# Kernel optimization log

Hardware: AMD Instinct MI355X
Metric: run time of the kernel (lower is better)

## Reference

```python
import jax, jax.numpy as jnp
import numpy as np
from jax import lax

B, S, H = 2, 1024, 1024
I = 512            # moe_intermediate_size
E = 32             # n_routed_experts
TOP_K = 4
N_GROUP = 4
TOPK_GROUP = 2
SCALE = 2.5        # routed_scaling_factor
N_SHARED = 2
SH_I = I * N_SHARED


def setup_inputs() -> dict:
    key = jax.random.key(0)
    ks = jax.random.split(key, 10)
    std = 0.02
    return {
        "hidden_states": jax.random.normal(ks[0], (B, S, H), jnp.float32),
        "router_weight": jax.random.normal(ks[1], (E, H), jnp.float32) * std,
        "router_bias": jnp.zeros((E,), jnp.float32),
        "gate_w": jax.random.normal(ks[2], (E, I, H), jnp.float32) * std,
        "up_w": jax.random.normal(ks[3], (E, I, H), jnp.float32) * std,
        "down_w": jax.random.normal(ks[4], (E, H, I), jnp.float32) * std,
        "shared_gate_w": jax.random.normal(ks[5], (SH_I, H), jnp.float32) * std,
        "shared_up_w": jax.random.normal(ks[6], (SH_I, H), jnp.float32) * std,
        "shared_down_w": jax.random.normal(ks[7], (H, SH_I), jnp.float32) * std,
    }


def _route(tokens, router_weight, router_bias):
    # tokens: [T, H] -> topk_idx [T, K] int, topk_weight [T, K] f32
    logits = tokens.astype(jnp.float32) @ router_weight.astype(jnp.float32).T  # [T, E]
    scores = jax.nn.sigmoid(logits)
    sfc = scores + router_bias[None, :]
    T = tokens.shape[0]
    # group scores: sum of top-2 per group
    grp = sfc.reshape(T, N_GROUP, E // N_GROUP)
    group_scores = lax.top_k(grp, 2)[0].sum(-1)                 # [T, n_group]
    _, gidx = lax.top_k(group_scores, TOPK_GROUP)               # [T, topk_group]
    gmask = jax.nn.one_hot(gidx, N_GROUP, dtype=sfc.dtype).sum(1)  # [T, n_group]
    smask = jnp.broadcast_to(gmask[:, :, None], (T, N_GROUP, E // N_GROUP)).reshape(T, E)
    tmp = jnp.where(smask > 0, sfc, 0.0)
    _, topk_idx = lax.top_k(tmp, TOP_K)                         # [T, K]
    topk_w = jnp.take_along_axis(scores, topk_idx, axis=1)
    topk_w = topk_w / (topk_w.sum(-1, keepdims=True) + 1e-20)   # norm_topk_prob
    topk_w = topk_w * SCALE
    return topk_idx, topk_w


def reference(hidden_states, router_weight, router_bias, gate_w, up_w, down_w,
              shared_gate_w, shared_up_w, shared_down_w):
    tokens = hidden_states.reshape(-1, H)                       # [T, H]
    topk_idx, topk_w = _route(tokens, router_weight, router_bias)
    # dense all-expert SwiGLU
    gate_vals = jax.nn.silu(jnp.einsum('th,eih->tei', tokens, gate_w))
    up_vals = jnp.einsum('th,eih->tei', tokens, up_w)
    hidden_vals = gate_vals * up_vals                           # [T, E, I]
    expert_out = jnp.einsum('tei,ehi->teh', hidden_vals, down_w)  # [T, E, H]
    sel = jnp.take_along_axis(expert_out, topk_idx[:, :, None], axis=1)  # [T, K, H]
    mixed = (sel * topk_w[:, :, None].astype(sel.dtype)).sum(1)
    mixed = mixed.reshape(hidden_states.shape)
    # shared experts (dense SwiGLU MLP)
    sg = jax.nn.silu(jnp.einsum('bsh,ih->bsi', hidden_states, shared_gate_w))
    su = jnp.einsum('bsh,ih->bsi', hidden_states, shared_up_w)
    shared = jnp.einsum('bsi,hi->bsh', sg * su, shared_down_w)
    return mixed + shared
```

## Files before the change

### kernel.cpp

```cpp
#include <hip/hip_runtime.h>
#include <hip/hip_bf16.h>
#include <math.h>

#define HD 1024
#define ID 512
#define NE 32
#define NT 2048
#define NG 4
#define SHI 1024
#define SCALE 2.5f

#define BN 64
#define BK 32
#define LDA 40
#define NCV 4

typedef __bf16 bf16_t;
typedef __attribute__((ext_vector_type(8))) __bf16 bf16x8;
typedef __attribute__((ext_vector_type(4))) __bf16 bf16x4;
typedef __attribute__((ext_vector_type(4))) float f32x4;

__device__ __forceinline__ void gld16(const bf16_t* g, bf16_t* l) {
    __builtin_amdgcn_global_load_lds(
        (__attribute__((address_space(1))) void*)g,
        (__attribute__((address_space(3))) void*)l,
        16, 0, 0);
}

__device__ __forceinline__ void cvt16(const float* __restrict__ src, bf16_t* __restrict__ dst) {
    float4 a0 = ((const float4*)src)[0], a1 = ((const float4*)src)[1];
    float4 a2 = ((const float4*)src)[2], a3 = ((const float4*)src)[3];
    bf16x8 o0, o1;
    o0[0]=(__bf16)a0.x; o0[1]=(__bf16)a0.y; o0[2]=(__bf16)a0.z; o0[3]=(__bf16)a0.w;
    o0[4]=(__bf16)a1.x; o0[5]=(__bf16)a1.y; o0[6]=(__bf16)a1.z; o0[7]=(__bf16)a1.w;
    o1[0]=(__bf16)a2.x; o1[1]=(__bf16)a2.y; o1[2]=(__bf16)a2.z; o1[3]=(__bf16)a2.w;
    o1[4]=(__bf16)a3.x; o1[5]=(__bf16)a3.y; o1[6]=(__bf16)a3.z; o1[7]=(__bf16)a3.w;
    ((bf16x8*)dst)[0] = o0;
    ((bf16x8*)dst)[1] = o1;
}

__global__ void __launch_bounds__(256) convert_A(
    const float* __restrict__ g, const float* __restrict__ u,
    const float* __restrict__ sg, const float* __restrict__ su,
    const float* __restrict__ hs, bf16_t* __restrict__ dst,
    float* __restrict__ outz)
{
    const long long UG = (long long)NE * ID * HD / 16;
    const long long US = (long long)SHI * HD / 16;
    const long long UH = (long long)NT * HD / 16;
    const long long TOTC = 2 * UG + 2 * US + UH;
    const long long TOT = TOTC + UH;
    for (long long c = blockIdx.x * 256LL + threadIdx.x; c < TOT;
         c += (long long)gridDim.x * 256LL) {
        if (c >= TOTC) {
            long long r = c - TOTC;
            float4 z = {0.f, 0.f, 0.f, 0.f};
            float4* p = (float4*)(outz + r * 16);
            p[0] = z; p[1] = z; p[2] = z; p[3] = z;
            continue;
        }
        const float* src;
        long long r = c;
        if (r < UG)                   src = g  + r * 16;
        else if ((r -= UG) < UG)      src = u  + r * 16;
        else if ((r -= UG) < US)      src = sg + r * 16;
        else if ((r -= US) < US)      src = su + r * 16;
        else { r -= US;               src = hs + r * 16; }
        cvt16(src, dst + c * 16);
    }
}

#define LTOK 8
#define LKC 64
__global__ void __launch_bounds__(256) logits_kernel(
    const float* __restrict__ hs, const float* __restrict__ rw,
    float* __restrict__ logits, int* __restrict__ counts)
{
    if (blockIdx.x == 0 && threadIdx.x < NE) counts[threadIdx.x] = 0;

    __shared__ float Xs[LTOK][68];
    __shared__ float Ws[NE][65];

    int tid = threadIdx.x;
    int t0 = blockIdx.x * LTOK;
    int tslot = tid >> 5, ecol = tid & 31;
    float acc = 0.f;

    for (int k0 = 0; k0 < HD; k0 += LKC) {
        if (tid < 128) {
            int row = tid >> 4, q = tid & 15;
            float4 v = *(const float4*)(hs + (size_t)(t0 + row) * HD + k0 + q * 4);
            *(float4*)(&Xs[row][q * 4]) = v;
        }
        #pragma unroll
        for (int i = 0; i < 8; ++i) {
            int idx = i * 256 + tid;
            int e = idx >> 6, kk = idx & 63;
            Ws[e][kk] = rw[(size_t)e * HD + k0 + kk];
        }
        __syncthreads();
        #pragma unroll 8
        for (int kk = 0; kk < LKC; ++kk)
            acc += Xs[tslot][kk] * Ws[ecol][kk];
        __syncthreads();
    }
    logits[(size_t)(t0 + tslot) * NE + ecol] = acc;
}

__global__ void __launch_bounds__(256) topk_kernel(
    const float* __restrict__ logits, const float* __restrict__ rb,
    float* __restrict__ topkw, int* __restrict__ counts, int* __restrict__ lists)
{
    int t = blockIdx.x * 256 + threadIdx.x;
    if (t >= NT) return;

    float scores[NE], sfc[NE], tmp[NE];
    #pragma unroll
    for (int e = 0; e < NE; ++e) {
        float l = logits[(size_t)t * NE + e];
        float s = 1.f / (1.f + __expf(-l));
        scores[e] = s;
        sfc[e] = s + rb[e];
    }
    float gs[NG];
    #pragma unroll
    for (int g = 0; g < NG; ++g) {
        float m1 = -1e30f, m2 = -1e30f;
        #pragma unroll
        for (int j = 0; j < 8; ++j) {
            float v = sfc[g * 8 + j];
            if (v > m1) { m2 = m1; m1 = v; } else if (v > m2) m2 = v;
        }
        gs[g] = m1 + m2;
    }
    int g1 = 0;
    #pragma unroll
    for (int g = 1; g < NG; ++g) if (gs[g] > gs[g1]) g1 = g;
    int g2 = -1;
    #pragma unroll
    for (int g = 0; g < NG; ++g) {
        if (g == g1) continue;
        if (g2 < 0 || gs[g] > gs[g2]) g2 = g;
    }
    #pragma unroll
    for (int e = 0; e < NE; ++e) {
        int g = e >> 3;
        tmp[e] = (g == g1 || g == g2) ? sfc[e] : 0.0f;
    }
    int idx[4]; float wk[4]; float wsum = 0.f;
    #pragma unroll
    for (int k = 0; k < 4; ++k) {
        int best = 0; float bv = -1e30f;
        #pragma unroll
        for (int e = 0; e < NE; ++e) if (tmp[e] > bv) { bv = tmp[e]; best = e; }
        idx[k] = best; tmp[best] = -1e30f;
        wk[k] = scores[best]; wsum += wk[k];
    }
    float inv = SCALE / (wsum + 1e-20f);
    #pragma unroll
    for (int k = 0; k < 4; ++k) {
        int p = t * 4 + k;
        topkw[p] = wk[k] * inv;
        int e = idx[k];
        int pos = atomicAdd(&counts[e], 1);
        lists[e * NT + pos] = p;
    }
}


__global__ void __launch_bounds__(256) gateup_all(
    const bf16_t* __restrict__ hs_b,
    const bf16_t* __restrict__ wg_b, const bf16_t* __restrict__ wu_b,
    const bf16_t* __restrict__ sg_b, const bf16_t* __restrict__ su_b,
    bf16_t* __restrict__ hr, bf16_t* __restrict__ hsh,
    const int* __restrict__ lists, const int* __restrict__ counts,
    const float* __restrict__ dwf, const float* __restrict__ sdwf,
    bf16_t* __restrict__ dstB)
{
    int bx = blockIdx.x, mtb = blockIdx.y, zz = blockIdx.z;
    int tid = threadIdx.x;

    if (bx >= 34) {
        const long long UD = (long long)NE * HD * ID / 16;
        const long long USD = (long long)HD * SHI / 16;
        const long long TOT = UD + USD;
        long long c = (((long long)(bx - 34) * 16 + mtb) * 8 + zz) * 256 + tid;
        const long long stride = (long long)NCV * 128 * 256;
        for (; c < TOT; c += stride) {
            const float* src = (c < UD) ? (dwf + c * 16) : (sdwf + (c - UD) * 16);
            cvt16(src, dstB + c * 16);
        }
        return;
    }

    constexpr int BMT = 128, NB = 64;
    constexpr int AU = 2, MT = 4;

    int cnt, ntb, ND;
    const bf16_t *wg, *wu;
    bf16_t* hout;
    const int* rlist = nullptr;
    if (bx < 32) {
        int e = bx; cnt = counts[e];
        if (mtb * BMT >= cnt) return;
        ntb = zz;
        wg = wg_b + (size_t)e * ID * HD;
        wu = wu_b + (size_t)e * ID * HD;
        hout = hr; ND = ID;
        rlist = lists + e * NT;
    } else {
        cnt = NT;
        ntb = (bx - 32) * 8 + zz;
        wg = sg_b; wu = su_b;
        hout = hsh; ND = SHI;
    }

    __shared__ __align__(16) bf16_t As[2][BMT * BK];
    __shared__ __align__(16) bf16_t Bgs[2][NB * BK];
    __shared__ __align__(16) bf16_t Bus[2][NB * BK];
    __shared__ int rowid[BMT];

    if (tid < BMT) {
        int gm = mtb * BMT + tid;
        int mm = gm < cnt ? gm : cnt - 1;
        rowid[tid] = rlist ? rlist[mm] : mm;
    }
    __syncthreads();

    int lane = tid & 63;
    int w = tid >> 6;
    int wm = w & 1, wn = w >> 1;
    int lrow = lane & 15, quad = lane >> 4, chunkL = lane & 3;

    const bf16_t* asrc[AU];
    #pragma unroll
    for (int i = 0; i < AU; ++i) {
        int row = (w * AU + i) * 16 + (lane >> 2);
        int tok = rlist ? (rowid[row] >> 2) : rowid[row];
        int ch = chunkL ^ ((row >> 1) & 3);
        asrc[i] = hs_b + (size_t)tok * HD + ch * 8;
    }
    int nrow = w * 16 + (lane >> 2);
    int nch = chunkL ^ ((nrow >> 1) & 3);
    const bf16_t* bgsrc = wg + (size_t)(ntb * NB + nrow) * HD + nch * 8;
    const bf16_t* busrc = wu + (size_t)(ntb * NB + nrow) * HD + nch * 8;

    int aoff[MT], goff[2];
    #pragma unroll
    for (int mt = 0; mt < MT; ++mt) {
        int row = wm * (BMT / 2) + mt * 16 + lrow;
        aoff[mt] = row * BK + (quad ^ ((row >> 1) & 3)) * 8;
    }
    #pragma unroll
    for (int nt = 0; nt < 2; ++nt) {
        int row = wn * 32 + nt * 16 + lrow;
        goff[nt] = row * BK + (quad ^ ((row >> 1) & 3)) * 8;
    }

    f32x4 accg[MT][2], accu[MT][2];
    #pragma unroll
    for (int i = 0; i < MT; ++i)
        #pragma unroll
        for (int j = 0; j < 2; ++j) { accg[i][j] = (f32x4){0,0,0,0}; accu[i][j] = (f32x4){0,0,0,0}; }

    auto stage = [&](int buf, int k) {
        #pragma unroll
        for (int i = 0; i < AU; ++i)
            gld16(asrc[i] + k, &As[buf][(w * AU + i) * 512]);
        gld16(bgsrc + k, &Bgs[buf][w * 512]);
        gld16(busrc + k, &Bus[buf][w * 512]);
    };
    auto compute = [&](int buf) {
        bf16x8 af[MT], bg[2], bu[2];
        #pragma unroll
        for (int mt = 0; mt < MT; ++mt) af[mt] = *(const bf16x8*)(&As[buf][aoff[mt]]);
        #pragma unroll
        for (int nt = 0; nt < 2; ++nt) {
            bg[nt] = *(const bf16x8*)(&Bgs[buf][goff[nt]]);
            bu[nt] = *(const bf16x8*)(&Bus[buf][goff[nt]]);
        }
        #pragma unroll
        for (int mt = 0; mt < MT; ++mt)
            #pragma unroll
            for (int nt = 0; nt < 2; ++nt) {
                accg[mt][nt] = __builtin_amdgcn_mfma_f32_16x16x32_bf16(af[mt], bg[nt], accg[mt][nt], 0, 0, 0);
                accu[mt][nt] = __builtin_amdgcn_mfma_f32_16x16x32_bf16(af[mt], bu[nt], accu[mt][nt], 0, 0, 0);
            }
    };

    stage(0, 0);
    __syncthreads();
    int buf = 0;
    for (int k0 = BK; k0 < HD; k0 += BK) {
        stage(buf ^ 1, k0);
        compute(buf);
        __syncthreads();
        buf ^= 1;
    }
    compute(buf);

    #pragma unroll
    for (int mt = 0; mt < MT; ++mt)
        #pragma unroll
        for (int r = 0; r < 4; ++r) {
            int row_local = wm * (BMT / 2) + mt * 16 + quad * 4 + r;
            int gm = mtb * BMT + row_local;
            if (gm >= cnt) continue;
            int p = rowid[row_local];
            #pragma unroll
            for (int nt = 0; nt < 2; ++nt) {
                int col = ntb * NB + wn * 32 + nt * 16 + lrow;
                float gv = accg[mt][nt][r], uv = accu[mt][nt][r];
                float h = (gv / (1.f + __expf(-gv))) * uv;
                hout[(size_t)p * ND + col] = (__bf16)h;
            }
        }
}

__global__ void __launch_bounds__(256) down_all(
    const bf16_t* __restrict__ hr, const bf16_t* __restrict__ hsh,
    const bf16_t* __restrict__ wd_b, const bf16_t* __restrict__ sd_b,
    float* __restrict__ out,
    const int* __restrict__ lists, const int* __restrict__ counts,
    const float* __restrict__ topkw)
{
    int bx = blockIdx.x, mtb = blockIdx.y, zz = blockIdx.z;
    int tid = threadIdx.x;

    constexpr int BMT = 128, NB = 64;
    constexpr int AU = 2, MT = 4;

    int cnt, ntb, KD;
    const bf16_t *Hin, *wd;
    const int* rlist = nullptr;
    bool routed;
    if (bx < 64) {
        int e = bx >> 1; cnt = counts[e];
        if (mtb * BMT >= cnt) return;
        ntb = (bx & 1) * 8 + zz;
        Hin = hr; wd = wd_b + (size_t)e * HD * ID; KD = ID;
        rlist = lists + e * NT;
        routed = true;
    } else {
        cnt = NT;
        ntb = (bx - 64) * 8 + zz;
        Hin = hsh; wd = sd_b; KD = SHI;
        routed = false;
    }

    __shared__ __align__(16) bf16_t As[2][BMT * BK];
    __shared__ __align__(16) bf16_t Ws[2][NB * BK];
    __shared__ int rowid[BMT];

    if (tid < BMT) {
        int gm = mtb * BMT + tid;
        int mm = gm < cnt ? gm : cnt - 1;
        rowid[tid] = rlist ? rlist[mm] : mm;
    }
    __syncthreads();

    int lane = tid & 63;
    int w = tid >> 6;
    int wm = w & 1, wn = w >> 1;
    int lrow = lane & 15, quad = lane >> 4, chunkL = lane & 3;

    const bf16_t* asrc[AU];
    #pragma unroll
    for (int i = 0; i < AU; ++i) {
        int row = (w * AU + i) * 16 + (lane >> 2);
        int ch = chunkL ^ ((row >> 1) & 3);
        asrc[i] = Hin + (size_t)rowid[row] * KD + ch * 8;
    }
    int nrow = w * 16 + (lane >> 2);
    int nch = chunkL ^ ((nrow >> 1) & 3);
    const bf16_t* wsrc = wd + (size_t)(ntb * NB + nrow) * KD + nch * 8;

    int aoff[MT], woff[2];
    #pragma unroll
    for (int mt = 0; mt < MT; ++mt) {
        int row = wm * (BMT / 2) + mt * 16 + lrow;
        aoff[mt] = row * BK + (quad ^ ((row >> 1) & 3)) * 8;
    }
    #pragma unroll
    for (int nt = 0; nt < 2; ++nt) {
        int row = wn * 32 + nt * 16 + lrow;
        woff[nt] = row * BK + (quad ^ ((row >> 1) & 3)) * 8;
    }

    f32x4 acc[MT][2];
    #pragma unroll
    for (int i = 0; i < MT; ++i)
        #pragma unroll
        for (int j = 0; j < 2; ++j) acc[i][j] = (f32x4){0,0,0,0};

    auto stage = [&](int buf, int k) {
        #pragma unroll
        for (int i = 0; i < AU; ++i)
            gld16(asrc[i] + k, &As[buf][(w * AU + i) * 512]);
        gld16(wsrc + k, &Ws[buf][w * 512]);
    };
    auto compute = [&](int buf) {
        bf16x8 af[MT], br[2];
        #pragma unroll
        for (int mt = 0; mt < MT; ++mt) af[mt] = *(const bf16x8*)(&As[buf][aoff[mt]]);
        #pragma unroll
        for (int nt = 0; nt < 2; ++nt) br[nt] = *(const bf16x8*)(&Ws[buf][woff[nt]]);
        #pragma unroll
        for (int mt = 0; mt < MT; ++mt)
            #pragma unroll
            for (int nt = 0; nt < 2; ++nt)
                acc[mt][nt] = __builtin_amdgcn_mfma_f32_16x16x32_bf16(af[mt], br[nt], acc[mt][nt], 0, 0, 0);
    };

    stage(0, 0);
    __syncthreads();
    int buf = 0;
    for (int k0 = BK; k0 < KD; k0 += BK) {
        stage(buf ^ 1, k0);
        compute(buf);
        __syncthreads();
        buf ^= 1;
    }
    compute(buf);

    #pragma unroll
    for (int mt = 0; mt < MT; ++mt)
        #pragma unroll
        for (int r = 0; r < 4; ++r) {
            int row_local = wm * (BMT / 2) + mt * 16 + quad * 4 + r;
            int gm = mtb * BMT + row_local;
            if (gm >= cnt) continue;
            int p = rowid[row_local];
            #pragma unroll
            for (int nt = 0; nt < 2; ++nt) {
                int col = ntb * NB + wn * 32 + nt * 16 + lrow;
                float val = acc[mt][nt][r];
                if (routed) {
                    float wgt = topkw[p];
                    atomicAdd(&out[(size_t)(p >> 2) * HD + col], wgt * val);
                } else {
                    atomicAdd(&out[(size_t)p * HD + col], val);
                }
            }
        }
}


__device__ inline bf16x4 cvt4(float4 v) {
    bf16x4 r;
    r[0] = (__bf16)v.x; r[1] = (__bf16)v.y; r[2] = (__bf16)v.z; r[3] = (__bf16)v.w;
    return r;
}

template<bool EXPERT, int ND, int BMT>
__global__ void __launch_bounds__(256) gateup_mfma(
    const float* __restrict__ X, const float* __restrict__ Wg,
    const float* __restrict__ Wu, bf16_t* __restrict__ Hout,
    const int* __restrict__ lists, const int* __restrict__ counts)
{
    int e = 0, cnt = NT;
    const float* wg = Wg; const float* wu = Wu;
    if (EXPERT) {
        e = blockIdx.x; cnt = counts[e];
        wg = Wg + (size_t)e * ND * HD;
        wu = Wu + (size_t)e * ND * HD;
    }
    int mtb = blockIdx.y, ntb = blockIdx.z;
    if (mtb * BMT >= cnt) return;

    __shared__ __align__(16) bf16_t As[BMT * LDA];
    __shared__ __align__(16) bf16_t Bgs[BN * LDA];
    __shared__ __align__(16) bf16_t Bus[BN * LDA];
    __shared__ int rowid[BMT];

    int tid = threadIdx.x;
    if (tid < BMT) {
        int gm = mtb * BMT + tid;
        int mm = gm < cnt ? gm : cnt - 1;
        rowid[tid] = EXPERT ? lists[e * NT + mm] : mm;
    }
    __syncthreads();

    constexpr int AR = (BMT * BK) / (256 * 4);
    constexpr int BR = (BN * BK) / (256 * 4);
    constexpr int MT = BMT / 32;

    int lane = tid & 63;
    int w = tid >> 6;
    int wm = w & 1, wn = w >> 1;
    int lrow = lane & 15, quad = lane >> 4;

    f32x4 accg[MT][2], accu[MT][2];
    #pragma unroll
    for (int i = 0; i < MT; ++i)
        #pragma unroll
        for (int j = 0; j < 2; ++j) { accg[i][j] = (f32x4){0,0,0,0}; accu[i][j] = (f32x4){0,0,0,0}; }

    float4 pa[AR], pbg[BR], pbu[BR];

    #pragma unroll
    for (int r = 0; r < AR; ++r) {
        int idx = r * 256 + tid;
        int row = idx >> 3, kq = idx & 7;
        int tok = EXPERT ? (rowid[row] >> 2) : rowid[row];
        pa[r] = *(const float4*)(X + (size_t)tok * HD + kq * 4);
    }
    #pragma unroll
    for (int r = 0; r < BR; ++r) {
        int idx = r * 256 + tid;
        int n = idx >> 3, kq = idx & 7;
        size_t off = (size_t)(ntb * BN + n) * HD + kq * 4;
        pbg[r] = *(const float4*)(wg + off);
        pbu[r] = *(const float4*)(wu + off);
    }

    for (int k0 = 0; k0 < HD; k0 += BK) {
        #pragma unroll
        for (int r = 0; r < AR; ++r) {
            int idx = r * 256 + tid;
            int row = idx >> 3, kq = idx & 7;
            *(bf16x4*)(As + row * LDA + kq * 4) = cvt4(pa[r]);
        }
        #pragma unroll
        for (int r = 0; r < BR; ++r) {
            int idx = r * 256 + tid;
            int n = idx >> 3, kq = idx & 7;
            *(bf16x4*)(Bgs + n * LDA + kq * 4) = cvt4(pbg[r]);
            *(bf16x4*)(Bus + n * LDA + kq * 4) = cvt4(pbu[r]);
        }
        __syncthreads();

        int k1 = k0 + BK;
        if (k1 < HD) {
            #pragma unroll
            for (int r = 0; r < AR; ++r) {
                int idx = r * 256 + tid;
                int row = idx >> 3, kq = idx & 7;
                int tok = EXPERT ? (rowid[row] >> 2) : rowid[row];
                pa[r] = *(const float4*)(X + (size_t)tok * HD + k1 + kq * 4);
            }
            #pragma unroll
            for (int r = 0; r < BR; ++r) {
                int idx = r * 256 + tid;
                int n = idx >> 3, kq = idx & 7;
                size_t off = (size_t)(ntb * BN + n) * HD + k1 + kq * 4;
                pbg[r] = *(const float4*)(wg + off);
                pbu[r] = *(const float4*)(wu + off);
            }
        }

        bf16x8 af[MT], bg[2], bu[2];
        #pragma unroll
        for (int mt = 0; mt < MT; ++mt)
            af[mt] = *(const bf16x8*)(As + (wm * (BMT / 2) + mt * 16 + lrow) * LDA + quad * 8);
        #pragma unroll
        for (int nt = 0; nt < 2; ++nt) {
            bg[nt] = *(const bf16x8*)(Bgs + (wn * 32 + nt * 16 + lrow) * LDA + quad * 8);
            bu[nt] = *(const bf16x8*)(Bus + (wn * 32 + nt * 16 + lrow) * LDA + quad * 8);
        }
        #pragma unroll
        for (int mt = 0; mt < MT; ++mt)
            #pragma unroll
            for (int nt = 0; nt < 2; ++nt) {
                accg[mt][nt] = __builtin_amdgcn_mfma_f32_16x16x32_bf16(af[mt], bg[nt], accg[mt][nt], 0, 0, 0);
                accu[mt][nt] = __builtin_amdgcn_mfma_f32_16x16x32_bf16(af[mt], bu[nt], accu[mt][nt], 0, 0, 0);
            }
        __syncthreads();
    }

    #pragma unroll
    for (int mt = 0; mt < MT; ++mt)
        #pragma unroll
        for (int r = 0; r < 4; ++r) {
            int row_local = wm * (BMT / 2) + mt * 16 + quad * 4 + r;
            int gm = mtb * BMT + row_local;
            if (gm >= cnt) continue;
            int p = rowid[row_local];
            #pragma unroll
            for (int nt = 0; nt < 2; ++nt) {
                int col = ntb * BN + wn * 32 + nt * 16 + lrow;
                float g = accg[mt][nt][r], u = accu[mt][nt][r];
                float h = (g / (1.f + __expf(-g))) * u;
                Hout[(size_t)p * ND + col] = (__bf16)h;
            }
        }
}

template<bool EXPERT, int KD, int BMT>
__global__ void __launch_bounds__(256) down_mfma(
    const bf16_t* __restrict__ Hin, const float* __restrict__ Wd,
    float* __restrict__ out, const int* __restrict__ lists,
    const int* __restrict__ counts, const float* __restrict__ topkw)
{
    int e = 0, cnt = NT;
    const float* wd = Wd;
    if (EXPERT) {
        e = blockIdx.x; cnt = counts[e];
        wd = Wd + (size_t)e * HD * KD;
    }
    int mtb = blockIdx.y, ntb = blockIdx.z;
    if (mtb * BMT >= cnt) return;

    __shared__ __align__(16) bf16_t As[BMT * LDA];
    __shared__ __align__(16) bf16_t Ws[BN * LDA];
    __shared__ int rowid[BMT];

    int tid = threadIdx.x;
    if (tid < BMT) {
        int gm = mtb * BMT + tid;
        int mm = gm < cnt ? gm : cnt - 1;
        rowid[tid] = EXPERT ? lists[e * NT + mm] : mm;
    }
    __syncthreads();

    constexpr int ARH = (BMT * BK / 8) / 256;
    constexpr int BR = (BN * BK) / (256 * 4);
    constexpr int MT = BMT / 32;

    int lane = tid & 63;
    int w = tid >> 6;
    int wm = w & 1, wn = w >> 1;
    int lrow = lane & 15, quad = lane >> 4;

    f32x4 acc[MT][2];
    #pragma unroll
    for (int i = 0; i < MT; ++i)
        #pragma unroll
        for (int j = 0; j < 2; ++j) acc[i][j] = (f32x4){0,0,0,0};

    bf16x8 pa[ARH];
    float4 pw[BR];

    #pragma unroll
    for (int r = 0; r < ARH; ++r) {
        int idx = r * 256 + tid;
        int row = idx >> 2, c = idx & 3;
        pa[r] = *(const bf16x8*)(Hin + (size_t)rowid[row] * KD + c * 8);
    }
    #pragma unroll
    for (int r = 0; r < BR; ++r) {
        int idx = r * 256 + tid;
        int n = idx >> 3, kq = idx & 7;
        pw[r] = *(const float4*)(wd + (size_t)(ntb * BN + n) * KD + kq * 4);
    }

    for (int k0 = 0; k0 < KD; k0 += BK) {
        #pragma unroll
        for (int r = 0; r < ARH; ++r) {
            int idx = r * 256 + tid;
            int row = idx >> 2, c = idx & 3;
            *(bf16x8*)(As + row * LDA + c * 8) = pa[r];
        }
        #pragma unroll
        for (int r = 0; r < BR; ++r) {
            int idx = r * 256 + tid;
            int n = idx >> 3, kq = idx & 7;
            *(bf16x4*)(Ws + n * LDA + kq * 4) = cvt4(pw[r]);
        }
        __syncthreads();

        int k1 = k0 + BK;
        if (k1 < KD) {
            #pragma unroll
            for (int r = 0; r < ARH; ++r) {
                int idx = r * 256 + tid;
                int row = idx >> 2, c = idx & 3;
                pa[r] = *(const bf16x8*)(Hin + (size_t)rowid[row] * KD + k1 + c * 8);
            }
            #pragma unroll
            for (int r = 0; r < BR; ++r) {
                int idx = r * 256 + tid;
                int n = idx >> 3, kq = idx & 7;
                pw[r] = *(const float4*)(wd + (size_t)(ntb * BN + n) * KD + k1 + kq * 4);
            }
        }

        bf16x8 af[MT], bfr[2];
        #pragma unroll
        for (int mt = 0; mt < MT; ++mt)
            af[mt] = *(const bf16x8*)(As + (wm * (BMT / 2) + mt * 16 + lrow) * LDA + quad * 8);
        #pragma unroll
        for (int nt = 0; nt < 2; ++nt)
            bfr[nt] = *(const bf16x8*)(Ws + (wn * 32 + nt * 16 + lrow) * LDA + quad * 8);
        #pragma unroll
        for (int mt = 0; mt < MT; ++mt)
            #pragma unroll
            for (int nt = 0; nt < 2; ++nt)
                acc[mt][nt] = __builtin_amdgcn_mfma_f32_16x16x32_bf16(af[mt], bfr[nt], acc[mt][nt], 0, 0, 0);
        __syncthreads();
    }

    #pragma unroll
    for (int mt = 0; mt < MT; ++mt)
        #pragma unroll
        for (int r = 0; r < 4; ++r) {
            int row_local = wm * (BMT / 2) + mt * 16 + quad * 4 + r;
            int gm = mtb * BMT + row_local;
            if (gm >= cnt) continue;
            int p = rowid[row_local];
            #pragma unroll
            for (int nt = 0; nt < 2; ++nt) {
                int col = ntb * BN + wn * 32 + nt * 16 + lrow;
                float val = acc[mt][nt][r];
                if (EXPERT) {
                    float wgt = topkw[p];
                    atomicAdd(&out[(size_t)(p >> 2) * HD + col], wgt * val);
                } else {
                    out[(size_t)p * HD + col] = val;
                }
            }
        }
}

extern "C" void kernel_launch(void* const* d_in, const int* in_sizes, int n_in,
                              void* d_out, int out_size, void* d_ws, size_t ws_size,
                              hipStream_t stream) {
    const float* hs  = (const float*)d_in[0];
    const float* rw  = (const float*)d_in[1];
    const float* rb  = (const float*)d_in[2];
    const float* gw  = (const float*)d_in[3];
    const float* uw  = (const float*)d_in[4];
    const float* dw  = (const float*)d_in[5];
    const float* sgw = (const float*)d_in[6];
    const float* suw = (const float*)d_in[7];
    const float* sdw = (const float*)d_in[8];
    float* out = (float*)d_out;
    char* ws = (char*)d_ws;

    constexpr size_t MIR_A = 2 * (size_t)NE * ID * HD + 2 * (size_t)SHI * HD + (size_t)NT * HD;
    constexpr size_t MIR_B = (size_t)NE * ID * HD + (size_t)SHI * HD;
    constexpr size_t HR_E  = (size_t)NT * 4 * ID;
    constexpr size_t HSH_E = (size_t)NT * SHI;
    constexpr size_t REQ_WS = (size_t)(1 << 20) + (MIR_A + MIR_B + HR_E + HSH_E) * 2;

    if (ws_size >= REQ_WS) {
        int*    counts = (int*)ws;
        float*  topkw  = (float*)(ws + 1024);
        int*    lists  = (int*)(ws + 1024 + 32768);
        float*  logits = (float*)(ws + 1024 + 32768 + 262144);

        bf16_t* mir  = (bf16_t*)(ws + (1 << 20));
        bf16_t* wg_b = mir;
        bf16_t* wu_b = wg_b + (size_t)NE * ID * HD;
        bf16_t* sg_b = wu_b + (size_t)NE * ID * HD;
        bf16_t* su_b = sg_b + (size_t)SHI * HD;
        bf16_t* hs_b = su_b + (size_t)SHI * HD;
        bf16_t* wd_b = hs_b + (size_t)NT * HD;
        bf16_t* sd_b = wd_b + (size_t)NE * ID * HD;
        bf16_t* hr   = sd_b + (size_t)SHI * HD;
        bf16_t* hsh  = hr + HR_E;

        logits_kernel<<<NT / LTOK, 256, 0, stream>>>(hs, rw, logits, counts);
        topk_kernel<<<NT / 256, 256, 0, stream>>>(logits, rb, topkw, counts, lists);
        convert_A<<<2048, 256, 0, stream>>>(gw, uw, sgw, suw, hs, mir, out);
        gateup_all<<<dim3(34 + NCV, 16, 8), 256, 0, stream>>>(
            hs_b, wg_b, wu_b, sg_b, su_b, hr, hsh, lists, counts, dw, sdw, wd_b);
        down_all<<<dim3(66, 16, 8), 256, 0, stream>>>(
            hr, hsh, wd_b, sd_b, out, lists, counts, topkw);
    } else {
        int*    counts = (int*)ws;
        float*  topkw  = (float*)(ws + 128);
        int*    lists  = (int*)(ws + 128 + 32768);
        float*  logits = (float*)(ws + 128 + 32768 + 262144);
        bf16_t* hbuf   = (bf16_t*)(ws + 128 + 32768 + 262144 + 262144);

        logits_kernel<<<NT / LTOK, 256, 0, stream>>>(hs, rw, logits, counts);
        topk_kernel<<<NT / 256, 256, 0, stream>>>(logits, rb, topkw, counts, lists);

        gateup_mfma<false, SHI, 64><<<dim3(1, NT / 64, SHI / BN), 256, 0, stream>>>(
            hs, sgw, suw, hbuf, nullptr, nullptr);
        down_mfma<false, SHI, 64><<<dim3(1, NT / 64, HD / BN), 256, 0, stream>>>(
            hbuf, sdw, out, nullptr, nullptr, nullptr);

        gateup_mfma<true, ID, 128><<<dim3(NE, NT / 128, ID / BN), 256, 0, stream>>>(
            hs, gw, uw, hbuf, lists, counts);
        down_mfma<true, ID, 128><<<dim3(NE, NT / 128, HD / BN), 256, 0, stream>>>(
            hbuf, dw, out, lists, counts, topkw);
    }
}
```

Before: 395.6 us.

## Triple-buffer GEMM staging with vmcnt-based sync and widen fp32-to-bf16 conversion

Both grouped GEMM kernels now keep three LDS stages and run two tiles ahead of compute. A single barrier per iteration is paired with an explicit s_waitcnt vmcnt that waits only for the oldest outstanding direct-to-LDS loads, replacing the double buffer that needed a full __syncthreads drain. Separately, the weight/activation conversion kernel now handles 32 floats per thread with nontemporal loads, which cuts loop overhead and avoids polluting the cache. In exchange, the GEMM kernels use more LDS, which may lower occupancy, and correctness depends on the hand-counted vmcnt values (4 and 3) matching the number of loads each stage issues.

Result: slower. 432.4 us (+9.3%).

```diff
diff --git a/kernel.cpp b/kernel.cpp
--- a/kernel.cpp
+++ b/kernel.cpp
@@ -26,6 +26,12 @@
         (__attribute__((address_space(3))) void*)l,
         16, 0, 0);
 }
+
+#define PIPE_SYNC(vm) do { \
+    asm volatile("s_waitcnt vmcnt(" #vm ") lgkmcnt(0)" ::: "memory"); \
+    __builtin_amdgcn_s_barrier(); \
+    asm volatile("" ::: "memory"); \
+} while (0)
 
 __device__ __forceinline__ void cvt16(const float* __restrict__ src, bf16_t* __restrict__ dst) {
     float4 a0 = ((const float4*)src)[0], a1 = ((const float4*)src)[1];
@@ -39,15 +45,30 @@
     ((bf16x8*)dst)[1] = o1;
 }
 
+__device__ __forceinline__ void cvt32nt(const float* __restrict__ src, bf16_t* __restrict__ dst) {
+    const f32x4* s4 = (const f32x4*)src;
+    f32x4 a[8];
+    #pragma unroll
+    for (int i = 0; i < 8; ++i) a[i] = __builtin_nontemporal_load(s4 + i);
+    #pragma unroll
+    for (int i = 0; i < 4; ++i) {
+        f32x4 lo = a[2*i], hi = a[2*i+1];
+        bf16x8 o;
+        o[0]=(__bf16)lo[0]; o[1]=(__bf16)lo[1]; o[2]=(__bf16)lo[2]; o[3]=(__bf16)lo[3];
+        o[4]=(__bf16)hi[0]; o[5]=(__bf16)hi[1]; o[6]=(__bf16)hi[2]; o[7]=(__bf16)hi[3];
+        ((bf16x8*)dst)[i] = o;
+    }
+}
+
 __global__ void __launch_bounds__(256) convert_A(
     const float* __restrict__ g, const float* __restrict__ u,
     const float* __restrict__ sg, const float* __restrict__ su,
     const float* __restrict__ hs, bf16_t* __restrict__ dst,
     float* __restrict__ outz)
 {
-    const long long UG = (long long)NE * ID * HD / 16;
-    const long long US = (long long)SHI * HD / 16;
-    const long long UH = (long long)NT * HD / 16;
+    const long long UG = (long long)NE * ID * HD / 32;
+    const long long US = (long long)SHI * HD / 32;
+    const long long UH = (long long)NT * HD / 32;
     const long long TOTC = 2 * UG + 2 * US + UH;
     const long long TOT = TOTC + UH;
     for (long long c = blockIdx.x * 256LL + threadIdx.x; c < TOT;
@@ -55,18 +76,19 @@
         if (c >= TOTC) {
             long long r = c - TOTC;
             float4 z = {0.f, 0.f, 0.f, 0.f};
-            float4* p = (float4*)(outz + r * 16);
-            p[0] = z; p[1] = z; p[2] = z; p[3] = z;
+            float4* p = (float4*)(outz + r * 32);
+            #pragma unroll
+            for (int i = 0; i < 8; ++i) p[i] = z;
             continue;
         }
         const float* src;
         long long r = c;
-        if (r < UG)                   src = g  + r * 16;
-        else if ((r -= UG) < UG)      src = u  + r * 16;
-        else if ((r -= UG) < US)      src = sg + r * 16;
-        else if ((r -= US) < US)      src = su + r * 16;
-        else { r -= US;               src = hs + r * 16; }
-        cvt16(src, dst + c * 16);
+        if (r < UG)                   src = g  + r * 32;
+        else if ((r -= UG) < UG)      src = u  + r * 32;
+        else if ((r -= UG) < US)      src = sg + r * 32;
+        else if ((r -= US) < US)      src = su + r * 32;
+        else { r -= US;               src = hs + r * 32; }
+        cvt32nt(src, dst + c * 32);
     }
 }
 
@@ -195,6 +217,7 @@
 
     constexpr int BMT = 128, NB = 64;
     constexpr int AU = 2, MT = 4;
+    constexpr int NS = HD / BK;
 
     int cnt, ntb, ND;
     const bf16_t *wg, *wu;
@@ -215,9 +238,9 @@
         hout = hsh; ND = SHI;
     }
 
-    __shared__ __align__(16) bf16_t As[2][BMT * BK];
-    __shared__ __align__(16) bf16_t Bgs[2][NB * BK];
-    __shared__ __align__(16) bf16_t Bus[2][NB * BK];
+    __shared__ __align__(16) bf16_t As[3][BMT * BK];
+    __shared__ __align__(16) bf16_t Bgs[3][NB * BK];
+    __shared__ __align__(16) bf16_t Bus[3][NB * BK];
     __shared__ int rowid[BMT];
 
     if (tid < BMT) {
@@ -289,15 +312,14 @@
     };
 
     stage(0, 0);
-    __syncthreads();
-    int buf = 0;
-    for (int k0 = BK; k0 < HD; k0 += BK) {
-        stage(buf ^ 1, k0);
-        compute(buf);
-        __syncthreads();
-        buf ^= 1;
-    }
-    compute(buf);
+    stage(1, BK);
+    for (int s = 0; s < NS - 1; ++s) {
+        PIPE_SYNC(4);
+        if (s + 2 < NS) stage((s + 2) % 3, (s + 2) * BK);
+        compute(s % 3);
+    }
+    PIPE_SYNC(0);
+    compute((NS - 1) % 3);
 
     #pragma unroll
     for (int mt = 0; mt < MT; ++mt)
@@ -348,8 +370,8 @@
         routed = false;
     }
 
-    __shared__ __align__(16) bf16_t As[2][BMT * BK];
-    __shared__ __align__(16) bf16_t Ws[2][NB * BK];
+    __shared__ __align__(16) bf16_t As[3][BMT * BK];
+    __shared__ __align__(16) bf16_t Ws[3][NB * BK];
     __shared__ int rowid[BMT];
 
     if (tid < BMT) {
@@ -412,16 +434,16 @@
                 acc[mt][nt] = __builtin_amdgcn_mfma_f32_16x16x32_bf16(af[mt], br[nt], acc[mt][nt], 0, 0, 0);
     };
 
+    int NS = KD / BK;
     stage(0, 0);
-    __syncthreads();
-    int buf = 0;
-    for (int k0 = BK; k0 < KD; k0 += BK) {
-        stage(buf ^ 1, k0);
-        compute(buf);
-        __syncthreads();
-        buf ^= 1;
-    }
-    compute(buf);
+    stage(1, BK);
+    for (int s = 0; s < NS - 1; ++s) {
+        PIPE_SYNC(3);
+        if (s + 2 < NS) stage((s + 2) % 3, (s + 2) * BK);
+        compute(s % 3);
+    }
+    PIPE_SYNC(0);
+    compute((NS - 1) % 3);
 
     #pragma unroll
     for (int mt = 0; mt < MT; ++mt)
```
